# Performance work log

Hardware: AMD Instinct MI355X
Metric: run time of the kernel (lower is better)

The kernel has to match this reference:

```python
import jax, jax.numpy as jnp
import numpy as np

N_HEAD = 12

def _rotate_half(x):
    # interleaved rotation: (-x1, x0, -x3, x2, ...)
    x_even = x[..., ::2]
    x_odd = x[..., 1::2]
    return jnp.stack((-x_odd, x_even), axis=-1).reshape(x.shape)

def _rope_tables(T, D, dtype):
    inv_freq = 1.0 / (10000.0 ** (jnp.arange(0, D, 2, dtype=jnp.float32) / D))
    freqs = jnp.arange(T, dtype=jnp.float32)[:, None] * inv_freq[None, :]  # [T, D/2]
    cos = jnp.repeat(jnp.cos(freqs), 2, axis=-1).astype(dtype)  # [T, D]
    sin = jnp.repeat(jnp.sin(freqs), 2, axis=-1).astype(dtype)
    return cos, sin

def setup_inputs() -> dict:
    key = jax.random.key(0)
    ks = jax.random.split(key, 5)
    B, T, C = 8, 1024, 768
    return {
        "x": jax.random.normal(ks[0], (B, T, C), dtype=jnp.float32),
        "W_attn": jax.random.normal(ks[1], (C, 3 * C), dtype=jnp.float32) * (C ** -0.5),
        "b_attn": jax.random.normal(ks[2], (3 * C,), dtype=jnp.float32) * 0.02,
        "W_proj": jax.random.normal(ks[3], (C, C), dtype=jnp.float32) * (C ** -0.5),
        "b_proj": jax.random.normal(ks[4], (C,), dtype=jnp.float32) * 0.02,
    }

def reference(x, W_attn, b_attn, W_proj, b_proj):
    B, T, C = x.shape
    H = N_HEAD
    D = C // H
    qkv = x @ W_attn + b_attn  # [B, T, 3C]
    q, k, v = jnp.split(qkv, 3, axis=-1)
    # [B, H, T, D]
    q = q.reshape(B, T, H, D).transpose(0, 2, 1, 3)
    k = k.reshape(B, T, H, D).transpose(0, 2, 1, 3)
    v = v.reshape(B, T, H, D).transpose(0, 2, 1, 3)
    cos, sin = _rope_tables(T, D, x.dtype)  # [T, D]
    q = q * cos + _rotate_half(q) * sin
    k = k * cos + _rotate_half(k) * sin
    att = jnp.einsum('bhqd,bhkd->bhqk', q, k) * (D ** -0.5)
    causal = jnp.tril(jnp.ones((T, T), dtype=bool))
    att = jnp.where(causal, att, -jnp.inf)
    att = jax.nn.softmax(att, axis=-1)
    y = jnp.einsum('bhqk,bhkd->bhqd', att, v)  # [B, H, T, D]
    y = y.transpose(0, 2, 1, 3).reshape(B, T, C)
    return y @ W_proj + b_proj
```

## Files before the change

kernel.cpp:

```cpp
#include <hip/hip_runtime.h>
#include <hip/hip_bf16.h>
#include <cstdint>
#include <cstddef>

typedef __attribute__((ext_vector_type(8))) short frag8;
typedef __attribute__((ext_vector_type(4))) float facc4;

__device__ __forceinline__ float b2f(unsigned short u) {
  union { unsigned int i; float f; } v; v.i = ((unsigned int)u) << 16; return v.f;
}
__device__ __forceinline__ unsigned short f2b(float f) {
  union { float f; unsigned int i; } v; v.f = f;
  unsigned int u = v.i;
  unsigned int r = (u + 0x7fffu + ((u >> 16) & 1u)) >> 16;
  return (unsigned short)r;
}
__device__ __forceinline__ unsigned long long pk4(float a, float b, float c, float d) {
  union { __hip_bfloat162 h2[2]; unsigned long long u; } pk;
  pk.h2[0] = __float22bfloat162_rn(float2{a, b});
  pk.h2[1] = __float22bfloat162_rn(float2{c, d});
  return pk.u;
}


__global__ void cvt_f32_bf16_k(const float* __restrict__ in, unsigned short* __restrict__ out, int n8) {
  int i = blockIdx.x * blockDim.x + threadIdx.x;
  if (i >= n8) return;
  const float4* p = (const float4*)in + (size_t)i * 2;
  float4 a = p[0], b = p[1];
  union { unsigned short u[8]; frag8 v; } o;
  o.u[0] = f2b(a.x); o.u[1] = f2b(a.y); o.u[2] = f2b(a.z); o.u[3] = f2b(a.w);
  o.u[4] = f2b(b.x); o.u[5] = f2b(b.y); o.u[6] = f2b(b.z); o.u[7] = f2b(b.w);
  *((frag8*)out + i) = o.v;
}

__global__ void transpose_cvt_k(const float* __restrict__ W, unsigned short* __restrict__ Wt, int R, int Cn) {
  __shared__ float tile[32][33];
  int tx = threadIdx.x, ty = threadIdx.y;
  int c = blockIdx.x * 32 + tx;
  #pragma unroll
  for (int i = 0; i < 32; i += 8)
    tile[ty + i][tx] = W[(size_t)(blockIdx.y * 32 + ty + i) * Cn + c];
  __syncthreads();
  int rr = blockIdx.y * 32 + tx;
  #pragma unroll
  for (int i = 0; i < 32; i += 8)
    Wt[(size_t)(blockIdx.x * 32 + ty + i) * R + rr] = f2b(tile[tx][ty + i]);
}

__global__ void rope_tables_k(float* __restrict__ cosT, float* __restrict__ sinT) {
  int id = blockIdx.x * 256 + threadIdx.x;
  int t = id >> 5, i = id & 31;
  float freq = powf(10000.0f, -(float)i * (1.0f / 32.0f));
  float a = (float)t * freq;
  cosT[id] = cosf(a);
  sinT[id] = sinf(a);
}

__global__ void rope_k(unsigned short* __restrict__ Q, unsigned short* __restrict__ Kb,
                       const float* __restrict__ cosT, const float* __restrict__ sinT) {
  int id = blockIdx.x * 256 + threadIdx.x;
  int i = id & 31;
  int t = (id >> 5) & 1023;
  int bh = id >> 15;
  size_t base = ((size_t)bh << 16) + (size_t)t * 64 + i * 2;
  float c = cosT[(t << 5) + i], s = sinT[(t << 5) + i];
  unsigned int* qp = (unsigned int*)(Q + base);
  unsigned int qu = *qp;
  float q0 = b2f(qu & 0xffffu), q1 = b2f(qu >> 16);
  *qp = (unsigned int)f2b(q0 * c - q1 * s) | ((unsigned int)f2b(q1 * c + q0 * s) << 16);
  unsigned int* kp = (unsigned int*)(Kb + base);
  unsigned int ku = *kp;
  float k0 = b2f(ku & 0xffffu), k1 = b2f(ku >> 16);
  *kp = (unsigned int)f2b(k0 * c - k1 * s) | ((unsigned int)f2b(k1 * c + k0 * s) << 16);
}


#define GLDK 72

template<int EPI>
__global__ __launch_bounds__(256)
void gemm128_k(const unsigned short* __restrict__ A, const unsigned short* __restrict__ Bt,
               const float* __restrict__ bias, float* __restrict__ outF,
               unsigned short* __restrict__ Qo, unsigned short* __restrict__ Ko,
               unsigned short* __restrict__ Vo, int M, int N, int K)
{
  __shared__ unsigned short As[128 * GLDK];
  __shared__ unsigned short Bs[128 * GLDK];
  const int tid = threadIdx.x;
  const int lane = tid & 63;
  const int w = tid >> 6, wm = w >> 1, wn = w & 1;
  const int g = lane >> 4, cL = lane & 15;

  const int nwg = gridDim.x * gridDim.y;
  const int flat = blockIdx.y * gridDim.x + blockIdx.x;
  const int cpx = nwg >> 3;
  const int swz = (flat & 7) * cpx + (flat >> 3);
  const int tM = (swz / gridDim.x) * 128, tN = (swz % gridDim.x) * 128;

  facc4 zero4 = {0.f, 0.f, 0.f, 0.f};
  facc4 acc[4][4];
  #pragma unroll
  for (int i = 0; i < 4; ++i)
    #pragma unroll
    for (int j = 0; j < 4; ++j) acc[i][j] = zero4;

  const int sr = tid >> 3;
  const int sc = (tid & 7) * 8;

  for (int k0 = 0; k0 < K; k0 += 64) {
    #pragma unroll
    for (int ch = 0; ch < 4; ++ch) {
      int r = sr + ch * 32;
      frag8 va = *(const frag8*)(A  + (size_t)(tM + r) * K + k0 + sc);
      frag8 vb = *(const frag8*)(Bt + (size_t)(tN + r) * K + k0 + sc);
      *(frag8*)(&As[r * GLDK + sc]) = va;
      *(frag8*)(&Bs[r * GLDK + sc]) = vb;
    }
    __syncthreads();
    #pragma unroll
    for (int kk = 0; kk < 2; ++kk) {
      frag8 af[4], bfr[4];
      #pragma unroll
      for (int i = 0; i < 4; ++i)
        af[i] = *(const frag8*)(&As[(wm * 64 + i * 16 + cL) * GLDK + kk * 32 + g * 8]);
      #pragma unroll
      for (int j = 0; j < 4; ++j)
        bfr[j] = *(const frag8*)(&Bs[(wn * 64 + j * 16 + cL) * GLDK + kk * 32 + g * 8]);
      #pragma unroll
      for (int i = 0; i < 4; ++i)
        #pragma unroll
        for (int j = 0; j < 4; ++j)
          acc[i][j] = __builtin_amdgcn_mfma_f32_16x16x32_bf16(af[i], bfr[j], acc[i][j], 0, 0, 0);
    }
    __syncthreads();
  }

  #pragma unroll
  for (int i = 0; i < 4; ++i) {
    #pragma unroll
    for (int j = 0; j < 4; ++j) {
      const int col = tN + wn * 64 + j * 16 + cL;
      const float bv = bias[col];
      if constexpr (EPI == 0) {
        const int sel = col / 768;
        const int cc = col - sel * 768;
        const int h = cc >> 6, d = cc & 63;
        #pragma unroll
        for (int r = 0; r < 4; ++r) {
          const int m = tM + wm * 64 + i * 16 + g * 4 + r;
          const float v = acc[i][j][r] + bv;
          const int b = m >> 10, t = m & 1023;
          const size_t hb = ((size_t)(b * 12 + h)) << 16;
          if (sel == 0)      Qo[hb + (size_t)t * 64 + d] = f2b(v * 0.125f);
          else if (sel == 1) Ko[hb + (size_t)t * 64 + d] = f2b(v);
          else               Vo[hb + ((size_t)d << 10) + t] = f2b(v);
        }
      } else {
        #pragma unroll
        for (int r = 0; r < 4; ++r) {
          const int m = tM + wm * 64 + i * 16 + g * 4 + r;
          outF[(size_t)m * N + col] = acc[i][j][r] + bv;
        }
      }
    }
  }
}


__device__ __forceinline__ void sm_pv(facc4 (&s)[4], frag8 (&vf)[2][4],
                                      unsigned short* PlW, int g, int cL,
                                      float& m, float& l, facc4 (&o)[4]) {
  float pm = fmaxf(fmaxf(fmaxf(s[0][0], s[0][1]), fmaxf(s[0][2], s[0][3])),
                   fmaxf(fmaxf(s[1][0], s[1][1]), fmaxf(s[1][2], s[1][3])));
  pm = fmaxf(pm, fmaxf(fmaxf(fmaxf(s[2][0], s[2][1]), fmaxf(s[2][2], s[2][3])),
                       fmaxf(fmaxf(s[3][0], s[3][1]), fmaxf(s[3][2], s[3][3]))));
  pm = fmaxf(pm, __shfl_xor(pm, 16));
  pm = fmaxf(pm, __shfl_xor(pm, 32));
  const float mn = fmaxf(m, pm);
  const float sc_ = __expf(m - mn);
  m = mn;
  float rs = 0.f;
  #pragma unroll
  for (int j = 0; j < 4; ++j)
    #pragma unroll
    for (int r = 0; r < 4; ++r) {
      const float p = __expf(s[j][r] - mn);
      s[j][r] = p;
      rs += p;
    }
  #pragma unroll
  for (int j = 0; j < 4; ++j)
    *(unsigned long long*)(&PlW[cL * GLDK + j * 16 + g * 4]) =
        pk4(s[j][0], s[j][1], s[j][2], s[j][3]);
  rs += __shfl_xor(rs, 16);
  rs += __shfl_xor(rs, 32);
  l = l * sc_ + rs;
  #pragma unroll
  for (int jd = 0; jd < 4; ++jd)
    #pragma unroll
    for (int r = 0; r < 4; ++r)
      o[jd][r] *= sc_;
  #pragma unroll
  for (int ks = 0; ks < 2; ++ks) {
    frag8 pa = *(const frag8*)(&PlW[cL * GLDK + ks * 32 + g * 8]);
    #pragma unroll
    for (int jd = 0; jd < 4; ++jd)
      o[jd] = __builtin_amdgcn_mfma_f32_16x16x32_bf16(vf[ks][jd], pa, o[jd], 0, 0, 0);
  }
}

__global__ __launch_bounds__(256, 3)
void attn_k(const unsigned short* __restrict__ Q, const unsigned short* __restrict__ Kb,
            const unsigned short* __restrict__ Vt, unsigned short* __restrict__ Y)
{
  __shared__ unsigned short Pl[8 * 16 * GLDK];
  const int tid = threadIdx.x, lane = tid & 63, w = tid >> 6;
  const int g = lane >> 4, cL = lane & 15;

  const int bid = blockIdx.x;
  const int xcd = bid & 7;
  const int slot = bid >> 3;
  const int bh = xcd + 8 * (slot % 12);
  const int x = slot / 12;
  const int qwA = (15 - x) * 64 + w * 16;
  const int qwB = x * 64 + w * 16;
  const int ntA = 16 - x, ntB = x + 1;
  const size_t hb = ((size_t)bh) << 16;

  frag8 qfA[2], qfB[2];
  #pragma unroll
  for (int ks = 0; ks < 2; ++ks) {
    qfA[ks] = *(const frag8*)(Q + hb + (size_t)(qwA + cL) * 64 + ks * 32 + g * 8);
    qfB[ks] = *(const frag8*)(Q + hb + (size_t)(qwB + cL) * 64 + ks * 32 + g * 8);
  }

  const unsigned short* Kp = Kb + hb + (size_t)cL * 64 + g * 8;
  const unsigned short* Vp = Vt + hb + (size_t)cL * 1024 + g * 8;
  unsigned short* PlA = &Pl[w * (16 * GLDK)];
  unsigned short* PlB = &Pl[(4 + w) * (16 * GLDK)];

  facc4 zero4 = {0.f, 0.f, 0.f, 0.f};
  facc4 oA[4], oB[4];
  #pragma unroll
  for (int jd = 0; jd < 4; ++jd) { oA[jd] = zero4; oB[jd] = zero4; }
  float mA = -1e30f, lA = 0.f, mB = -1e30f, lB = 0.f;

  frag8 kf[2][4];
  #pragma unroll
  for (int ks = 0; ks < 2; ++ks)
    #pragma unroll
    for (int j = 0; j < 4; ++j)
      kf[ks][j] = *(const frag8*)(Kp + (size_t)(j * 16) * 64 + ks * 32);

  for (int it = 0; it < ntA; ++it) {
    const int kv0 = it * 64;
    const bool doB = (it < ntB);
    facc4 sA[4], sB[4];
    #pragma unroll
    for (int j = 0; j < 4; ++j) { sA[j] = zero4; sB[j] = zero4; }
    #pragma unroll
    for (int ks = 0; ks < 2; ++ks)
      #pragma unroll
      for (int j = 0; j < 4; ++j)
        sA[j] = __builtin_amdgcn_mfma_f32_16x16x32_bf16(kf[ks][j], qfA[ks], sA[j], 0, 0, 0);
    if (doB) {
      #pragma unroll
      for (int ks = 0; ks < 2; ++ks)
        #pragma unroll
        for (int j = 0; j < 4; ++j)
          sB[j] = __builtin_amdgcn_mfma_f32_16x16x32_bf16(kf[ks][j], qfB[ks], sB[j], 0, 0, 0);
    }
    frag8 vf[2][4];
    #pragma unroll
    for (int ks = 0; ks < 2; ++ks)
      #pragma unroll
      for (int jd = 0; jd < 4; ++jd)
        vf[ks][jd] = *(const frag8*)(Vp + (size_t)(jd * 16) * 1024 + kv0 + ks * 32);
    if (it + 1 < ntA) {
      const int kn = (it + 1) * 64;
      #pragma unroll
      for (int ks = 0; ks < 2; ++ks)
        #pragma unroll
        for (int j = 0; j < 4; ++j)
          kf[ks][j] = *(const frag8*)(Kp + (size_t)(kn + j * 16) * 64 + ks * 32);
    }
    if (kv0 + 63 > qwA) {
      const int qrow = qwA + cL;
      #pragma unroll
      for (int j = 0; j < 4; ++j)
        #pragma unroll
        for (int r = 0; r < 4; ++r)
          if (kv0 + j * 16 + g * 4 + r > qrow) sA[j][r] = -1e30f;
    }
    if (doB && kv0 + 63 > qwB) {
      const int qrow = qwB + cL;
      #pragma unroll
      for (int j = 0; j < 4; ++j)
        #pragma unroll
        for (int r = 0; r < 4; ++r)
          if (kv0 + j * 16 + g * 4 + r > qrow) sB[j][r] = -1e30f;
    }
    sm_pv(sA, vf, PlA, g, cL, mA, lA, oA);
    if (doB) sm_pv(sB, vf, PlB, g, cL, mB, lB, oB);
  }

  const int b = bh / 12, h = bh - (bh / 12) * 12;
  const float invA = 1.0f / lA;
  const size_t yrowA = (size_t)(b * 1024 + qwA + cL) * 768 + h * 64;
  #pragma unroll
  for (int jd = 0; jd < 4; ++jd)
    *(unsigned long long*)(&Y[yrowA + jd * 16 + g * 4]) =
        pk4(oA[jd][0] * invA, oA[jd][1] * invA, oA[jd][2] * invA, oA[jd][3] * invA);
  const float invB = 1.0f / lB;
  const size_t yrowB = (size_t)(b * 1024 + qwB + cL) * 768 + h * 64;
  #pragma unroll
  for (int jd = 0; jd < 4; ++jd)
    *(unsigned long long*)(&Y[yrowB + jd * 16 + g * 4]) =
        pk4(oB[jd][0] * invB, oB[jd][1] * invB, oB[jd][2] * invB, oB[jd][3] * invB);
}


extern "C" void kernel_launch(void* const* d_in, const int* in_sizes, int n_in,
                              void* d_out, int out_size, void* d_ws, size_t ws_size,
                              hipStream_t stream) {
  const float* x      = (const float*)d_in[0];
  const float* W_attn = (const float*)d_in[1];
  const float* b_attn = (const float*)d_in[2];
  const float* W_proj = (const float*)d_in[3];
  const float* b_proj = (const float*)d_in[4];
  float* out = (float*)d_out;
  char* ws = (char*)d_ws;

  unsigned short* xb  = (unsigned short*)(ws);
  unsigned short* WtA = (unsigned short*)(ws + 12582912);
  unsigned short* WtP = (unsigned short*)(ws + 16121856);
  unsigned short* Qb  = (unsigned short*)(ws + 17301504);
  unsigned short* Kb  = (unsigned short*)(ws + 29884416);
  unsigned short* Vt  = (unsigned short*)(ws + 42467328);
  unsigned short* Yb  = (unsigned short*)(ws + 55050240);
  float* cosT = (float*)(ws + 67633152);
  float* sinT = (float*)(ws + 67764224);

  cvt_f32_bf16_k<<<3072, 256, 0, stream>>>(x, xb, 786432);
  transpose_cvt_k<<<dim3(72, 24), dim3(32, 8), 0, stream>>>(W_attn, WtA, 768, 2304);
  transpose_cvt_k<<<dim3(24, 24), dim3(32, 8), 0, stream>>>(W_proj, WtP, 768, 768);
  rope_tables_k<<<128, 256, 0, stream>>>(cosT, sinT);
  gemm128_k<0><<<dim3(18, 64), 256, 0, stream>>>(xb, WtA, b_attn, nullptr, Qb, Kb, Vt, 8192, 2304, 768);
  rope_k<<<12288, 256, 0, stream>>>(Qb, Kb, cosT, sinT);
  attn_k<<<768, 256, 0, stream>>>(Qb, Kb, Vt, Yb);
  gemm128_k<1><<<dim3(6, 64), 256, 0, stream>>>(Yb, WtP, b_proj, out, nullptr, nullptr, nullptr, 8192, 768, 768);
}
```

Before: 281.6 us.

## Fuse RoPE into QKV GEMM epilogue, use direct global-to-LDS loads, lazy softmax rescale

The standalone RoPE kernel is removed. Rotation is now applied in the QKV GEMM epilogue, using a lane-xor shuffle to fetch the paired element, which saves a full read-modify-write pass over Q and K. GEMM tile loads now use global_load_lds to copy straight into unpadded LDS tiles, skipping the register staging. That risks bank conflicts on the fragment reads, since the padding is gone. The attention softmax now rescales the output and running sum only when the block max exceeds the running max by more than a threshold, and MFMA sections get a raised wave priority via s_setprio.

```diff
diff --git a/kernel.cpp b/kernel.cpp
--- a/kernel.cpp
+++ b/kernel.cpp
@@ -20,6 +20,11 @@
   pk.h2[0] = __float22bfloat162_rn(float2{a, b});
   pk.h2[1] = __float22bfloat162_rn(float2{c, d});
   return pk.u;
+}
+__device__ __forceinline__ void gl_lds16(const unsigned short* g, unsigned short* l) {
+  __builtin_amdgcn_global_load_lds(
+      (const __attribute__((address_space(1))) void*)g,
+      (__attribute__((address_space(3))) void*)l, 16, 0, 0);
 }
 
 
@@ -57,39 +62,21 @@
   sinT[id] = sinf(a);
 }
 
-__global__ void rope_k(unsigned short* __restrict__ Q, unsigned short* __restrict__ Kb,
-                       const float* __restrict__ cosT, const float* __restrict__ sinT) {
-  int id = blockIdx.x * 256 + threadIdx.x;
-  int i = id & 31;
-  int t = (id >> 5) & 1023;
-  int bh = id >> 15;
-  size_t base = ((size_t)bh << 16) + (size_t)t * 64 + i * 2;
-  float c = cosT[(t << 5) + i], s = sinT[(t << 5) + i];
-  unsigned int* qp = (unsigned int*)(Q + base);
-  unsigned int qu = *qp;
-  float q0 = b2f(qu & 0xffffu), q1 = b2f(qu >> 16);
-  *qp = (unsigned int)f2b(q0 * c - q1 * s) | ((unsigned int)f2b(q1 * c + q0 * s) << 16);
-  unsigned int* kp = (unsigned int*)(Kb + base);
-  unsigned int ku = *kp;
-  float k0 = b2f(ku & 0xffffu), k1 = b2f(ku >> 16);
-  *kp = (unsigned int)f2b(k0 * c - k1 * s) | ((unsigned int)f2b(k1 * c + k0 * s) << 16);
-}
-
-
-#define GLDK 72
 
 template<int EPI>
 __global__ __launch_bounds__(256)
 void gemm128_k(const unsigned short* __restrict__ A, const unsigned short* __restrict__ Bt,
                const float* __restrict__ bias, float* __restrict__ outF,
                unsigned short* __restrict__ Qo, unsigned short* __restrict__ Ko,
-               unsigned short* __restrict__ Vo, int M, int N, int K)
+               unsigned short* __restrict__ Vo,
+               const float* __restrict__ cosT, const float* __restrict__ sinT,
+               int M, int N, int K)
 {
-  __shared__ unsigned short As[128 * GLDK];
-  __shared__ unsigned short Bs[128 * GLDK];
+  __shared__ unsigned short As[128 * 64];
+  __shared__ unsigned short Bs[128 * 64];
   const int tid = threadIdx.x;
   const int lane = tid & 63;
-  const int w = tid >> 6, wm = w >> 1, wn = w & 1;
+  const int wv = tid >> 6, wm = wv >> 1, wn = wv & 1;
   const int g = lane >> 4, cL = lane & 15;
 
   const int nwg = gridDim.x * gridDim.y;
@@ -105,17 +92,16 @@
     #pragma unroll
     for (int j = 0; j < 4; ++j) acc[i][j] = zero4;
 
-  const int sr = tid >> 3;
-  const int sc = (tid & 7) * 8;
+  const int srow = lane >> 3;
+  const int scol = (lane & 7) * 8;
 
   for (int k0 = 0; k0 < K; k0 += 64) {
     #pragma unroll
-    for (int ch = 0; ch < 4; ++ch) {
-      int r = sr + ch * 32;
-      frag8 va = *(const frag8*)(A  + (size_t)(tM + r) * K + k0 + sc);
-      frag8 vb = *(const frag8*)(Bt + (size_t)(tN + r) * K + k0 + sc);
-      *(frag8*)(&As[r * GLDK + sc]) = va;
-      *(frag8*)(&Bs[r * GLDK + sc]) = vb;
+    for (int i = 0; i < 4; ++i) {
+      const int chunk = wv * 4 + i;
+      const int row = chunk * 8 + srow;
+      gl_lds16(A  + (size_t)(tM + row) * K + k0 + scol, &As[chunk * 512]);
+      gl_lds16(Bt + (size_t)(tN + row) * K + k0 + scol, &Bs[chunk * 512]);
     }
     __syncthreads();
     #pragma unroll
@@ -123,10 +109,10 @@
       frag8 af[4], bfr[4];
       #pragma unroll
       for (int i = 0; i < 4; ++i)
-        af[i] = *(const frag8*)(&As[(wm * 64 + i * 16 + cL) * GLDK + kk * 32 + g * 8]);
+        af[i] = *(const frag8*)(&As[(wm * 64 + i * 16 + cL) * 64 + kk * 32 + g * 8]);
       #pragma unroll
       for (int j = 0; j < 4; ++j)
-        bfr[j] = *(const frag8*)(&Bs[(wn * 64 + j * 16 + cL) * GLDK + kk * 32 + g * 8]);
+        bfr[j] = *(const frag8*)(&Bs[(wn * 64 + j * 16 + cL) * 64 + kk * 32 + g * 8]);
       #pragma unroll
       for (int i = 0; i < 4; ++i)
         #pragma unroll
@@ -152,9 +138,16 @@
           const float v = acc[i][j][r] + bv;
           const int b = m >> 10, t = m & 1023;
           const size_t hb = ((size_t)(b * 12 + h)) << 16;
-          if (sel == 0)      Qo[hb + (size_t)t * 64 + d] = f2b(v * 0.125f);
-          else if (sel == 1) Ko[hb + (size_t)t * 64 + d] = f2b(v);
-          else               Vo[hb + ((size_t)d << 10) + t] = f2b(v);
+          if (sel < 2) {
+            const float vp = __shfl_xor(v, 1);
+            const float cs = cosT[(t << 5) + (d >> 1)];
+            const float sn = sinT[(t << 5) + (d >> 1)];
+            const float rot = v * cs + ((d & 1) ? vp * sn : -vp * sn);
+            if (sel == 0) Qo[hb + (size_t)t * 64 + d] = f2b(rot * 0.125f);
+            else          Ko[hb + (size_t)t * 64 + d] = f2b(rot);
+          } else {
+            Vo[hb + ((size_t)d << 10) + t] = f2b(v);
+          }
         }
       } else {
         #pragma unroll
@@ -167,6 +160,8 @@
   }
 }
 
+
+#define GLDK 72
 
 __device__ __forceinline__ void sm_pv(facc4 (&s)[4], frag8 (&vf)[2][4],
                                       unsigned short* PlW, int g, int cL,
@@ -177,15 +172,23 @@
                        fmaxf(fmaxf(s[3][0], s[3][1]), fmaxf(s[3][2], s[3][3]))));
   pm = fmaxf(pm, __shfl_xor(pm, 16));
   pm = fmaxf(pm, __shfl_xor(pm, 32));
-  const float mn = fmaxf(m, pm);
-  const float sc_ = __expf(m - mn);
-  m = mn;
+  if (!__all(pm <= m + 8.0f)) {
+    const float mn = fmaxf(m, pm);
+    const float sc_ = __expf(m - mn);
+    m = mn;
+    l *= sc_;
+    #pragma unroll
+    for (int jd = 0; jd < 4; ++jd)
+      #pragma unroll
+      for (int r = 0; r < 4; ++r)
+        o[jd][r] *= sc_;
+  }
   float rs = 0.f;
   #pragma unroll
   for (int j = 0; j < 4; ++j)
     #pragma unroll
     for (int r = 0; r < 4; ++r) {
-      const float p = __expf(s[j][r] - mn);
+      const float p = __expf(s[j][r] - m);
       s[j][r] = p;
       rs += p;
     }
@@ -195,12 +198,8 @@
         pk4(s[j][0], s[j][1], s[j][2], s[j][3]);
   rs += __shfl_xor(rs, 16);
   rs += __shfl_xor(rs, 32);
-  l = l * sc_ + rs;
-  #pragma unroll
-  for (int jd = 0; jd < 4; ++jd)
-    #pragma unroll
-    for (int r = 0; r < 4; ++r)
-      o[jd][r] *= sc_;
+  l += rs;
+  __builtin_amdgcn_s_setprio(1);
   #pragma unroll
   for (int ks = 0; ks < 2; ++ks) {
     frag8 pa = *(const frag8*)(&PlW[cL * GLDK + ks * 32 + g * 8]);
@@ -208,6 +207,7 @@
     for (int jd = 0; jd < 4; ++jd)
       o[jd] = __builtin_amdgcn_mfma_f32_16x16x32_bf16(vf[ks][jd], pa, o[jd], 0, 0, 0);
   }
+  __builtin_amdgcn_s_setprio(0);
 }
 
 __global__ __launch_bounds__(256, 3)
@@ -259,6 +259,7 @@
     facc4 sA[4], sB[4];
     #pragma unroll
     for (int j = 0; j < 4; ++j) { sA[j] = zero4; sB[j] = zero4; }
+    __builtin_amdgcn_s_setprio(1);
     #pragma unroll
     for (int ks = 0; ks < 2; ++ks)
       #pragma unroll
@@ -271,6 +272,7 @@
         for (int j = 0; j < 4; ++j)
           sB[j] = __builtin_amdgcn_mfma_f32_16x16x32_bf16(kf[ks][j], qfB[ks], sB[j], 0, 0, 0);
     }
+    __builtin_amdgcn_s_setprio(0);
     frag8 vf[2][4];
     #pragma unroll
     for (int ks = 0; ks < 2; ++ks)
@@ -342,12 +344,11 @@
   float* cosT = (float*)(ws + 67633152);
   float* sinT = (float*)(ws + 67764224);
 
+  rope_tables_k<<<128, 256, 0, stream>>>(cosT, sinT);
   cvt_f32_bf16_k<<<3072, 256, 0, stream>>>(x, xb, 786432);
   transpose_cvt_k<<<dim3(72, 24), dim3(32, 8), 0, stream>>>(W_attn, WtA, 768, 2304);
   transpose_cvt_k<<<dim3(24, 24), dim3(32, 8), 0, stream>>>(W_proj, WtP, 768, 768);
-  rope_tables_k<<<128, 256, 0, stream>>>(cosT, sinT);
-  gemm128_k<0><<<dim3(18, 64), 256, 0, stream>>>(xb, WtA, b_attn, nullptr, Qb, Kb, Vt, 8192, 2304, 768);
-  rope_k<<<12288, 256, 0, stream>>>(Qb, Kb, cosT, sinT);
+  gemm128_k<0><<<dim3(18, 64), 256, 0, stream>>>(xb, WtA, b_attn, nullptr, Qb, Kb, Vt, cosT, sinT, 8192, 2304, 768);
   attn_k<<<768, 256, 0, stream>>>(Qb, Kb, Vt, Yb);
-  gemm128_k<1><<<dim3(6, 64), 256, 0, stream>>>(Yb, WtP, b_proj, out, nullptr, nullptr, nullptr, 8192, 768, 768);
-}
+  gemm128_k<1><<<dim3(6, 64), 256, 0, stream>>>(Yb, WtP, b_proj, out, nullptr, nullptr, nullptr, nullptr, nullptr, 8192, 768, 768);
+}
```

Result: slower. 294.5 us (+4.6%).
